# Optimization experiments

Measured on AMD Instinct MI355X. Metric: run time of the kernel, lower is better.

Reference implementation:

```python
import jax, jax.numpy as jnp
import numpy as np

NUM_HEADS = 16
HIDDEN = 1024
B, S = 2, 2048


def setup_inputs() -> dict:
    key = jax.random.key(0)
    ks = jax.random.split(key, 14)
    D = HIDDEN
    scale = 1.0 / np.sqrt(D)
    inp = {
        "query": jax.random.normal(ks[0], (B, S, D), jnp.float32),
        "key_in": jax.random.normal(ks[1], (B, S, D), jnp.float32),
        "value": jax.random.normal(ks[2], (B, S, D), jnp.float32),
        "group_prob": jax.random.uniform(ks[3], (B, S, S), jnp.float32),
        "mask": jax.random.randint(ks[4], (B, S, S), 0, 2, jnp.int32),
        "wq_k": jax.random.normal(ks[5], (D, D), jnp.float32) * scale,
        "wq_b": jnp.zeros((D,), jnp.float32),
        "wk_k": jax.random.normal(ks[6], (D, D), jnp.float32) * scale,
        "wk_b": jnp.zeros((D,), jnp.float32),
        "wv_k": jax.random.normal(ks[7], (D, D), jnp.float32) * scale,
        "wv_b": jnp.zeros((D,), jnp.float32),
        "wo_k": jax.random.normal(ks[8], (D, D), jnp.float32) * scale,
        "wo_b": jnp.zeros((D,), jnp.float32),
    }
    return inp


def _split_heads(x, H):
    b, s, d = x.shape
    return x.reshape(b, s, H, d // H).transpose(0, 2, 1, 3)  # (B,H,S,dh)


def reference(query, key_in, value, group_prob, mask,
              wq_k, wq_b, wk_k, wk_b, wv_k, wv_b, wo_k, wo_b):
    H = NUM_HEADS
    dh = query.shape[-1] // H
    q = _split_heads(query @ wq_k + wq_b, H)
    k = _split_heads(key_in @ wk_k + wk_b, H)
    v = _split_heads(value @ wv_k + wv_b, H)
    # scaled dot-product logits (B,H,Sq,Sk)
    logits = jnp.einsum('bhqd,bhkd->bhqk', q, k) / jnp.sqrt(jnp.asarray(dh, q.dtype))
    neg = (1.0 - mask.astype(q.dtype)) * -1e9
    logits = logits + neg[:, None, :, :]
    attn = jax.nn.softmax(logits, axis=-1)
    # Tree Transformer modulation: post-softmax elementwise scale by group_prob
    attn = attn * group_prob[:, None, :, :]
    out = jnp.einsum('bhqk,bhkd->bhqd', attn, v)
    out = out.transpose(0, 2, 1, 3).reshape(query.shape[0], -1, H * dh)
    return out @ wo_k + wo_b
```

## Files before the change

### kernel.cpp

```cpp
#include <hip/hip_runtime.h>
#include <hip/hip_bf16.h>
#include <stdint.h>

#define B_ 2
#define S_ 2048
#define D_ 1024
#define H_ 16
#define DH 64

typedef __attribute__((ext_vector_type(4))) float f32x4;
typedef __attribute__((ext_vector_type(8))) short s16x8;
typedef __attribute__((ext_vector_type(4))) short s16x4;

__device__ inline short f2bf(float f) {
  union { float f; unsigned u; } v; v.f = f;
  unsigned r = (v.u + 0x7fffu + ((v.u >> 16) & 1u)) >> 16;
  return (short)r;
}

__device__ inline float bfbits_lo(unsigned u) {
  union { unsigned x; float f; } v; v.x = u << 16; return v.f;
}
__device__ inline float bfbits_hi(unsigned u) {
  union { unsigned x; float f; } v; v.x = u & 0xffff0000u; return v.f;
}

__device__ inline float exp2v(float x) {
  float r; asm("v_exp_f32 %0, %1" : "=v"(r) : "v"(x)); return r;
}
__device__ inline unsigned cvtpk(float a, float b) {
  unsigned r; asm("v_cvt_pk_bf16_f32 %0, %1, %2" : "=v"(r) : "v"(a), "v"(b));
  return r;
}

__global__ __launch_bounds__(256) void cvt3_f32_bf16(const float* __restrict__ a,
                                                     const float* __restrict__ b,
                                                     const float* __restrict__ c,
                                                     short* oa, short* ob, short* oc,
                                                     int n) {
  int z = blockIdx.y;
  const float* in = z == 0 ? a : (z == 1 ? b : c);
  short* out = z == 0 ? oa : (z == 1 ? ob : oc);
  int i = (blockIdx.x * 256 + threadIdx.x) * 4;
  if (i < n) {
    float4 v = *(const float4*)(in + i);
    s16x4 o;
    o.x = f2bf(v.x); o.y = f2bf(v.y); o.z = f2bf(v.z); o.w = f2bf(v.w);
    *(s16x4*)(out + i) = o;
  }
}

__global__ __launch_bounds__(256) void fuse_mgp(const int* __restrict__ mask,
                                                const float* __restrict__ gp,
                                                short* __restrict__ mgp, int n) {
  int i = (blockIdx.x * 256 + threadIdx.x) * 4;
  if (i < n) {
    int4 m = *(const int4*)(mask + i);
    float4 g = *(const float4*)(gp + i);
    short b0 = f2bf(g.x); if (!b0) b0 = (short)0x0080;
    short b1 = f2bf(g.y); if (!b1) b1 = (short)0x0080;
    short b2 = f2bf(g.z); if (!b2) b2 = (short)0x0080;
    short b3 = f2bf(g.w); if (!b3) b3 = (short)0x0080;
    s16x4 o;
    o.x = m.x ? b0 : 0;
    o.y = m.y ? b1 : 0;
    o.z = m.z ? b2 : 0;
    o.w = m.w ? b3 : 0;
    *(s16x4*)(mgp + i) = o;
  }
}

__global__ __launch_bounds__(256) void transpose_cvt4(
    const float* __restrict__ i0, const float* __restrict__ i1,
    const float* __restrict__ i2, const float* __restrict__ i3,
    short* o0, short* o1, short* o2, short* o3) {
  int z = blockIdx.z;
  const float* in = z == 0 ? i0 : (z == 1 ? i1 : (z == 2 ? i2 : i3));
  short* out = z == 0 ? o0 : (z == 1 ? o1 : (z == 2 ? o2 : o3));
  __shared__ float tile[32][33];
  int bx = blockIdx.x, by = blockIdx.y;
  int x = bx * 32 + threadIdx.x;
#pragma unroll
  for (int i = 0; i < 32; i += 8) {
    int y = by * 32 + threadIdx.y + i;
    tile[threadIdx.y + i][threadIdx.x] = in[(size_t)y * D_ + x];
  }
  __syncthreads();
  int ox = by * 32 + threadIdx.x;
#pragma unroll
  for (int i = 0; i < 32; i += 8) {
    int oy = bx * 32 + threadIdx.y + i;
    out[(size_t)oy * D_ + ox] = f2bf(tile[threadIdx.x][threadIdx.y + i]);
  }
}

__device__ inline void gload_lds16(const void* g, void* l) {
  __builtin_amdgcn_global_load_lds(
      (const __attribute__((address_space(1))) unsigned*)g,
      (__attribute__((address_space(3))) unsigned*)l, 16, 0, 0);
}

#define BM 128
#define BN 128
#define BK 32

__global__ __launch_bounds__(256) void gemm_bt3(
    const short* __restrict__ A0, const short* __restrict__ A1, const short* __restrict__ A2,
    const short* __restrict__ Bt0, const short* __restrict__ Bt1, const short* __restrict__ Bt2,
    const float* __restrict__ bs0, const float* __restrict__ bs1, const float* __restrict__ bs2,
    void* C0, void* C1, void* C2,
    short* __restrict__ vtout, int vtmode,
    int M, int N, int K, int f32out, float os0, float os1, float os2) {
  int z = blockIdx.y;
  const short* A = z == 0 ? A0 : (z == 1 ? A1 : A2);
  const short* Bt = z == 0 ? Bt0 : (z == 1 ? Bt1 : Bt2);
  const float* bias = z == 0 ? bs0 : (z == 1 ? bs1 : bs2);
  void* C = z == 0 ? C0 : (z == 1 ? C1 : C2);
  float oscale = z == 0 ? os0 : (z == 1 ? os1 : os2);

  __shared__ __align__(16) short As[BM * BK];
  __shared__ __align__(16) short Bs[BN * BK];
  int tid = threadIdx.x;
  int lane = tid & 63, wave = tid >> 6;
  int l15 = lane & 15, l4 = lane >> 4;
  int ntn = N / BN;
  int bid = blockIdx.x;
  bid = ((bid & 7) << 5) | (bid >> 3);
  int bm = bid / ntn, bn = bid % ntn;
  int row0 = bm * BM, col0 = bn * BN;
  int wm = (wave >> 1) * 64, wn = (wave & 1) * 64;

  f32x4 acc[4][4] = {};

  for (int k0 = 0; k0 < K; k0 += BK) {
    __syncthreads();
#pragma unroll
    for (int it = 0; it < 2; ++it) {
      int ch = it * 256 + tid;
      int r = ch >> 2, c = (ch & 3) * 8;
      int ldsbase = (it * 256 + wave * 64) * 8;
      gload_lds16(A + (size_t)(row0 + r) * K + k0 + c, &As[ldsbase]);
      gload_lds16(Bt + (size_t)(col0 + r) * K + k0 + c, &Bs[ldsbase]);
    }
    __syncthreads();
    s16x8 af[4], bf[4];
#pragma unroll
    for (int mf = 0; mf < 4; ++mf)
      af[mf] = *(const s16x8*)&As[(wm + mf * 16 + l15) * BK + l4 * 8];
#pragma unroll
    for (int nf = 0; nf < 4; ++nf)
      bf[nf] = *(const s16x8*)&Bs[(wn + nf * 16 + l15) * BK + l4 * 8];
#pragma unroll
    for (int mf = 0; mf < 4; ++mf)
#pragma unroll
      for (int nf = 0; nf < 4; ++nf)
        acc[mf][nf] = __builtin_amdgcn_mfma_f32_16x16x32_bf16(af[mf], bf[nf],
                                                              acc[mf][nf], 0, 0, 0);
  }

  if (vtmode && z == 2) {
    int b = row0 >> 11;
    int h = (col0 + wn) >> 6;
    int sbase = (row0 & (S_ - 1)) + wm + l4 * 4;
    short* vtb = vtout + ((size_t)(b * H_ + h) * DH) * S_;
#pragma unroll
    for (int nf = 0; nf < 4; ++nf) {
      int dh = nf * 16 + l15;
      float bv = bias[col0 + wn + dh];
#pragma unroll
      for (int mf = 0; mf < 4; ++mf) {
        uint2 o;
        o.x = cvtpk(acc[mf][nf][0] + bv, acc[mf][nf][1] + bv);
        o.y = cvtpk(acc[mf][nf][2] + bv, acc[mf][nf][3] + bv);
        *(uint2*)&vtb[(size_t)dh * S_ + sbase + mf * 16] = o;
      }
    }
    return;
  }

#pragma unroll
  for (int nf = 0; nf < 4; ++nf) {
    int gcol = col0 + wn + nf * 16 + l15;
    float bv = bias[gcol];
#pragma unroll
    for (int mf = 0; mf < 4; ++mf) {
#pragma unroll
      for (int r = 0; r < 4; ++r) {
        int grow = row0 + wm + mf * 16 + l4 * 4 + r;
        float v = (acc[mf][nf][r] + bv) * oscale;
        if (f32out)
          ((float*)C)[(size_t)grow * N + gcol] = v;
        else
          ((short*)C)[(size_t)grow * N + gcol] = f2bf(v);
      }
    }
  }
}

#define QB 128
#define NB 64
#define NTILES (S_ / NB)
#define M0_SHIFT 12.0f

__global__ __launch_bounds__(256, 3) void attn_fused(const short* __restrict__ Qp,
                                                     const short* __restrict__ Kp,
                                                     const short* __restrict__ VT,
                                                     const short* __restrict__ MGP,
                                                     short* __restrict__ ctx) {
  __shared__ __align__(16) short Ks[2][64 * 64];
  __shared__ __align__(16) short Vs[2][64 * 64];
  __shared__ __align__(16) short Ps[4][32 * 64];

  int tid = threadIdx.x, lane = tid & 63, wave = tid >> 6;
  int l15 = lane & 15, l4 = lane >> 4;
  int q0 = blockIdx.x * QB;
  int bh = blockIdx.y;
  int b = bh >> 4, h = bh & 15;
  int wq = wave * 32;

  const short* Qbase = Qp + (size_t)b * S_ * D_ + (size_t)h * DH;
  const short* Kbase = Kp + (size_t)b * S_ * D_ + (size_t)h * DH;
  const short* Vbase = VT + (size_t)(b * H_ + h) * DH * S_;
  const short* Mrow0 = MGP + (size_t)b * S_ * S_ + (size_t)(q0 + wq + l15) * S_ + l4 * 4;
  const short* Mrow1 = Mrow0 + (size_t)16 * S_;

  int i0 = tid, i1 = 256 + tid;
  int r0 = i0 >> 3, c0 = (i0 & 7) ^ (r0 & 7);
  int r1 = i1 >> 3, c1 = (i1 & 7) ^ (r1 & 7);
  int ldsA = wave * 512;
  int ldsB = 2048 + wave * 512;

#define STAGE(kv0, buf)                                                       \
  do {                                                                        \
    gload_lds16(Kbase + (size_t)((kv0) + r0) * D_ + c0 * 8, &Ks[buf][ldsA]);  \
    gload_lds16(Kbase + (size_t)((kv0) + r1) * D_ + c1 * 8, &Ks[buf][ldsB]);  \
    gload_lds16(Vbase + (size_t)r0 * S_ + (kv0) + c0 * 8, &Vs[buf][ldsA]);    \
    gload_lds16(Vbase + (size_t)r1 * S_ + (kv0) + c1 * 8, &Vs[buf][ldsB]);    \
  } while (0)

  s16x8 qf[2][2];
#pragma unroll
  for (int mf = 0; mf < 2; ++mf)
#pragma unroll
    for (int ks = 0; ks < 2; ++ks)
      qf[mf][ks] = *(const s16x8*)(Qbase + (size_t)(q0 + wq + mf * 16 + l15) * D_ +
                                   ks * 32 + l4 * 8);

  float lsum[2] = {0.f, 0.f};
  f32x4 oacc[2][4] = {};

  STAGE(0, 0);

  int q7 = l15 & 7;
  short* Pw = &Ps[wave][0];
  int prow[2] = {l15 * 64, (16 + l15) * 64};

  for (int t = 0; t < NTILES; ++t) {
    int buf = t & 1;
    int kvt = t * NB;

    uint2 g2[2][4];
#pragma unroll
    for (int nf = 0; nf < 4; ++nf) {
      g2[0][nf] = *(const uint2*)(Mrow0 + kvt + nf * 16);
      g2[1][nf] = *(const uint2*)(Mrow1 + kvt + nf * 16);
    }
    __builtin_amdgcn_sched_barrier(0);
    if (t + 1 < NTILES) {
      STAGE((t + 1) * NB, buf ^ 1);
      __builtin_amdgcn_sched_barrier(0);
      asm volatile("s_waitcnt vmcnt(12)" ::: "memory");
    } else {
      __builtin_amdgcn_sched_barrier(0);
      asm volatile("s_waitcnt vmcnt(8)" ::: "memory");
    }
    __builtin_amdgcn_s_barrier();
    __builtin_amdgcn_sched_barrier(0);

    f32x4 sacc[2][4] = {};
    __builtin_amdgcn_s_setprio(1);
#pragma unroll
    for (int nf = 0; nf < 4; ++nf) {
      int R = nf * 16 + l15;
#pragma unroll
      for (int ks = 0; ks < 2; ++ks) {
        s16x8 kf = *(const s16x8*)&Ks[buf][R * 64 + (((ks * 4 + l4) ^ q7) * 8)];
#pragma unroll
        for (int mf = 0; mf < 2; ++mf)
          sacc[mf][nf] = __builtin_amdgcn_mfma_f32_16x16x32_bf16(kf, qf[mf][ks],
                                                                 sacc[mf][nf], 0, 0, 0);
      }
    }
    __builtin_amdgcn_s_setprio(0);

    float ee[2][4][4];
#pragma unroll
    for (int mf = 0; mf < 2; ++mf)
#pragma unroll
      for (int nf = 0; nf < 4; ++nf)
#pragma unroll
        for (int r = 0; r < 4; ++r)
          ee[mf][nf][r] = exp2v(sacc[mf][nf][r] - M0_SHIFT);

    if (t + 1 < NTILES)
      asm volatile("s_waitcnt vmcnt(4)" ::: "memory");
    else
      asm volatile("s_waitcnt vmcnt(0)" ::: "memory");
    __builtin_amdgcn_sched_barrier(0);

#pragma unroll
    for (int mf = 0; mf < 2; ++mf) {
#pragma unroll
      for (int nf = 0; nf < 4; ++nf) {
        float gv0 = bfbits_lo(g2[mf][nf].x), gv1 = bfbits_hi(g2[mf][nf].x);
        float gv2 = bfbits_lo(g2[mf][nf].y), gv3 = bfbits_hi(g2[mf][nf].y);
        float e0 = ee[mf][nf][0], e1 = ee[mf][nf][1];
        float e2 = ee[mf][nf][2], e3 = ee[mf][nf][3];
        lsum[mf] += (gv0 != 0.f) ? e0 : 0.f;
        lsum[mf] += (gv1 != 0.f) ? e1 : 0.f;
        lsum[mf] += (gv2 != 0.f) ? e2 : 0.f;
        lsum[mf] += (gv3 != 0.f) ? e3 : 0.f;
        uint2 wp;
        wp.x = cvtpk(e0 * gv0, e1 * gv1);
        wp.y = cvtpk(e2 * gv2, e3 * gv3);
        int gr = ((nf * 2 + (l4 >> 1)) ^ q7) * 8 + (l4 & 1) * 4;
        *(uint2*)&Pw[prow[mf] + gr] = wp;
      }
    }

    __builtin_amdgcn_s_setprio(1);
#pragma unroll
    for (int ks = 0; ks < 2; ++ks) {
      s16x8 pa[2];
#pragma unroll
      for (int mf = 0; mf < 2; ++mf)
        pa[mf] = *(const s16x8*)&Pw[prow[mf] + (((ks * 4 + l4) ^ q7) * 8)];
#pragma unroll
      for (int df = 0; df < 4; ++df) {
        s16x8 vf = *(const s16x8*)&Vs[buf][(df * 16 + l15) * 64 +
                                           (((ks * 4 + l4) ^ q7) * 8)];
#pragma unroll
        for (int mf = 0; mf < 2; ++mf)
          oacc[mf][df] = __builtin_amdgcn_mfma_f32_16x16x32_bf16(vf, pa[mf],
                                                                 oacc[mf][df], 0, 0, 0);
      }
    }
    __builtin_amdgcn_s_setprio(0);

    asm volatile("s_waitcnt lgkmcnt(0)" ::: "memory");
    __builtin_amdgcn_s_barrier();
  }
#undef STAGE

#pragma unroll
  for (int mf = 0; mf < 2; ++mf) {
    float ls = lsum[mf];
    ls += __shfl_xor(ls, 16);
    ls += __shfl_xor(ls, 32);
    float inv = 1.f / ls;
    short* crow = ctx + ((size_t)(b * S_ + q0 + wq + mf * 16 + l15)) * D_ + h * DH;
#pragma unroll
    for (int df = 0; df < 4; ++df) {
      uint2 o;
      o.x = cvtpk(oacc[mf][df][0] * inv, oacc[mf][df][1] * inv);
      o.y = cvtpk(oacc[mf][df][2] * inv, oacc[mf][df][3] * inv);
      *(uint2*)(crow + df * 16 + l4 * 4) = o;
    }
  }
}

extern "C" void kernel_launch(void* const* d_in, const int* in_sizes, int n_in,
                              void* d_out, int out_size, void* d_ws, size_t ws_size,
                              hipStream_t stream) {
  const float* query = (const float*)d_in[0];
  const float* key_in = (const float*)d_in[1];
  const float* value = (const float*)d_in[2];
  const float* group_prob = (const float*)d_in[3];
  const int* mask = (const int*)d_in[4];
  const float* wq_k = (const float*)d_in[5];
  const float* wq_b = (const float*)d_in[6];
  const float* wk_k = (const float*)d_in[7];
  const float* wk_b = (const float*)d_in[8];
  const float* wv_k = (const float*)d_in[9];
  const float* wv_b = (const float*)d_in[10];
  const float* wo_k = (const float*)d_in[11];
  const float* wo_b = (const float*)d_in[12];
  float* out = (float*)d_out;

  short* ws = (short*)d_ws;
  const size_t NT = (size_t)B_ * S_ * D_;
  short* qbf = ws;
  short* kbf = qbf + NT;
  short* vbf = kbf + NT;
  short* wqt = vbf + NT;
  short* wkt = wqt + (size_t)D_ * D_;
  short* wvt = wkt + (size_t)D_ * D_;
  short* wot = wvt + (size_t)D_ * D_;
  short* qp = wot + (size_t)D_ * D_;
  short* kp = qp + NT;
  short* vt = kp + NT;
  short* ctx = vt + NT;
  short* mgp = ws;

  int nblk = (int)(NT / 4 / 256);
  cvt3_f32_bf16<<<dim3(nblk, 3), 256, 0, stream>>>(query, key_in, value,
                                                   qbf, kbf, vbf, (int)NT);

  dim3 tb(32, 8);
  transpose_cvt4<<<dim3(D_ / 32, D_ / 32, 4), tb, 0, stream>>>(
      wq_k, wk_k, wv_k, wo_k, wqt, wkt, wvt, wot);

  int M = B_ * S_;
  int gblocks = (M / BM) * (D_ / BN);
  const float QSCALE = 0.125f * 1.4426950408889634f;
  gemm_bt3<<<dim3(gblocks, 3), 256, 0, stream>>>(
      qbf, kbf, vbf, wqt, wkt, wvt, wq_b, wk_b, wv_b, qp, kp, nullptr,
      vt, 1, M, D_, D_, 0, QSCALE, 1.0f, 1.0f);

  int nmg = B_ * S_ * S_;
  fuse_mgp<<<nmg / 4 / 256, 256, 0, stream>>>(mask, group_prob, mgp, nmg);

  dim3 ag(S_ / QB, B_ * H_);
  attn_fused<<<ag, 256, 0, stream>>>(qp, kp, vt, mgp, ctx);

  gemm_bt3<<<dim3(gblocks, 1), 256, 0, stream>>>(
      ctx, ctx, ctx, wot, wot, wot, wo_b, wo_b, wo_b, out, out, out,
      nullptr, 0, M, D_, D_, 1, 1.0f, 1.0f, 1.0f);
}
```

Baseline: 175.8 us.

## Fuse fp32-to-bf16 input conversion into QKV GEMM and co-schedule mask fusion

Removes the separate input conversion kernel: the QKV GEMM now loads fp32 activations straight into LDS with an XOR swizzle and converts them to bf16 in registers before the MFMA. The mask/group_prob fusion runs as a fourth grid slice of the same launch, so it overlaps with the GEMM work and one launch disappears. The output GEMM becomes its own specialised kernel. In exchange the A tile in LDS is twice as large and each tile pays conversion instructions. The mgp slice only has gblocks blocks grid-striding over 8M elements, so it may become a long tail.

```diff
diff --git a/kernel.cpp b/kernel.cpp
--- a/kernel.cpp
+++ b/kernel.cpp
@@ -31,43 +31,6 @@
 __device__ inline unsigned cvtpk(float a, float b) {
   unsigned r; asm("v_cvt_pk_bf16_f32 %0, %1, %2" : "=v"(r) : "v"(a), "v"(b));
   return r;
-}
-
-__global__ __launch_bounds__(256) void cvt3_f32_bf16(const float* __restrict__ a,
-                                                     const float* __restrict__ b,
-                                                     const float* __restrict__ c,
-                                                     short* oa, short* ob, short* oc,
-                                                     int n) {
-  int z = blockIdx.y;
-  const float* in = z == 0 ? a : (z == 1 ? b : c);
-  short* out = z == 0 ? oa : (z == 1 ? ob : oc);
-  int i = (blockIdx.x * 256 + threadIdx.x) * 4;
-  if (i < n) {
-    float4 v = *(const float4*)(in + i);
-    s16x4 o;
-    o.x = f2bf(v.x); o.y = f2bf(v.y); o.z = f2bf(v.z); o.w = f2bf(v.w);
-    *(s16x4*)(out + i) = o;
-  }
-}
-
-__global__ __launch_bounds__(256) void fuse_mgp(const int* __restrict__ mask,
-                                                const float* __restrict__ gp,
-                                                short* __restrict__ mgp, int n) {
-  int i = (blockIdx.x * 256 + threadIdx.x) * 4;
-  if (i < n) {
-    int4 m = *(const int4*)(mask + i);
-    float4 g = *(const float4*)(gp + i);
-    short b0 = f2bf(g.x); if (!b0) b0 = (short)0x0080;
-    short b1 = f2bf(g.y); if (!b1) b1 = (short)0x0080;
-    short b2 = f2bf(g.z); if (!b2) b2 = (short)0x0080;
-    short b3 = f2bf(g.w); if (!b3) b3 = (short)0x0080;
-    s16x4 o;
-    o.x = m.x ? b0 : 0;
-    o.y = m.y ? b1 : 0;
-    o.z = m.z ? b2 : 0;
-    o.w = m.w ? b3 : 0;
-    *(s16x4*)(mgp + i) = o;
-  }
 }
 
 __global__ __launch_bounds__(256) void transpose_cvt4(
@@ -104,20 +67,135 @@
 #define BN 128
 #define BK 32
 
-__global__ __launch_bounds__(256) void gemm_bt3(
-    const short* __restrict__ A0, const short* __restrict__ A1, const short* __restrict__ A2,
+__global__ __launch_bounds__(256) void gemm_qkv(
+    const float* __restrict__ A0, const float* __restrict__ A1, const float* __restrict__ A2,
     const short* __restrict__ Bt0, const short* __restrict__ Bt1, const short* __restrict__ Bt2,
     const float* __restrict__ bs0, const float* __restrict__ bs1, const float* __restrict__ bs2,
-    void* C0, void* C1, void* C2,
-    short* __restrict__ vtout, int vtmode,
-    int M, int N, int K, int f32out, float os0, float os1, float os2) {
+    short* __restrict__ Cq, short* __restrict__ Ck, short* __restrict__ vtout,
+    const int* __restrict__ mask, const float* __restrict__ gp,
+    short* __restrict__ mgpout, int nmg,
+    int M, int N, int K, float os0) {
   int z = blockIdx.y;
-  const short* A = z == 0 ? A0 : (z == 1 ? A1 : A2);
+  if (z == 3) {
+    int i = (blockIdx.x * 256 + threadIdx.x) * 4;
+    int stride = gridDim.x * 256 * 4;
+    for (; i < nmg; i += stride) {
+      int4 m = *(const int4*)(mask + i);
+      float4 g = *(const float4*)(gp + i);
+      short b0 = f2bf(g.x); if (!b0) b0 = (short)0x0080;
+      short b1 = f2bf(g.y); if (!b1) b1 = (short)0x0080;
+      short b2 = f2bf(g.z); if (!b2) b2 = (short)0x0080;
+      short b3 = f2bf(g.w); if (!b3) b3 = (short)0x0080;
+      s16x4 o;
+      o.x = m.x ? b0 : 0;
+      o.y = m.y ? b1 : 0;
+      o.z = m.z ? b2 : 0;
+      o.w = m.w ? b3 : 0;
+      *(s16x4*)(mgpout + i) = o;
+    }
+    return;
+  }
+  const float* A = z == 0 ? A0 : (z == 1 ? A1 : A2);
   const short* Bt = z == 0 ? Bt0 : (z == 1 ? Bt1 : Bt2);
   const float* bias = z == 0 ? bs0 : (z == 1 ? bs1 : bs2);
-  void* C = z == 0 ? C0 : (z == 1 ? C1 : C2);
-  float oscale = z == 0 ? os0 : (z == 1 ? os1 : os2);
-
+  float oscale = z == 0 ? os0 : 1.0f;
+
+  __shared__ __align__(16) float As[BM * BK];
+  __shared__ __align__(16) short Bs[BN * BK];
+  int tid = threadIdx.x;
+  int lane = tid & 63, wave = tid >> 6;
+  int l15 = lane & 15, l4 = lane >> 4;
+  int ntn = N / BN;
+  int bid = blockIdx.x;
+  bid = ((bid & 7) << 5) | (bid >> 3);
+  int bm = bid / ntn, bn = bid % ntn;
+  int row0 = bm * BM, col0 = bn * BN;
+  int wm = (wave >> 1) * 64, wn = (wave & 1) * 64;
+  int q7 = l15 & 7;
+
+  f32x4 acc[4][4] = {};
+
+  for (int k0 = 0; k0 < K; k0 += BK) {
+    __syncthreads();
+#pragma unroll
+    for (int it = 0; it < 2; ++it) {
+      int ch = it * 256 + tid;
+      int r = ch >> 2, c = (ch & 3) * 8;
+      int ldsbase = (it * 256 + wave * 64) * 8;
+      gload_lds16(Bt + (size_t)(col0 + r) * K + k0 + c, &Bs[ldsbase]);
+    }
+#pragma unroll
+    for (int it = 0; it < 4; ++it) {
+      int ch = it * 256 + tid;
+      int r = ch >> 3, g = (ch & 7) ^ (r & 7);
+      int ldsbase = (it * 256 + wave * 64) * 4;
+      gload_lds16(A + (size_t)(row0 + r) * K + k0 + g * 4, &As[ldsbase]);
+    }
+    __syncthreads();
+    s16x8 af[4], bf[4];
+#pragma unroll
+    for (int mf = 0; mf < 4; ++mf) {
+      int row = wm + mf * 16 + l15;
+      f32x4 a0 = *(const f32x4*)&As[row * BK + (((2 * l4) ^ q7) * 4)];
+      f32x4 a1 = *(const f32x4*)&As[row * BK + (((2 * l4 + 1) ^ q7) * 4)];
+      union { unsigned w[4]; s16x8 v; } u;
+      u.w[0] = cvtpk(a0[0], a0[1]);
+      u.w[1] = cvtpk(a0[2], a0[3]);
+      u.w[2] = cvtpk(a1[0], a1[1]);
+      u.w[3] = cvtpk(a1[2], a1[3]);
+      af[mf] = u.v;
+    }
+#pragma unroll
+    for (int nf = 0; nf < 4; ++nf)
+      bf[nf] = *(const s16x8*)&Bs[(wn + nf * 16 + l15) * BK + l4 * 8];
+#pragma unroll
+    for (int mf = 0; mf < 4; ++mf)
+#pragma unroll
+      for (int nf = 0; nf < 4; ++nf)
+        acc[mf][nf] = __builtin_amdgcn_mfma_f32_16x16x32_bf16(af[mf], bf[nf],
+                                                              acc[mf][nf], 0, 0, 0);
+  }
+
+  if (z == 2) {
+    int b = row0 >> 11;
+    int h = (col0 + wn) >> 6;
+    int sbase = (row0 & (S_ - 1)) + wm + l4 * 4;
+    short* vtb = vtout + ((size_t)(b * H_ + h) * DH) * S_;
+#pragma unroll
+    for (int nf = 0; nf < 4; ++nf) {
+      int dh = nf * 16 + l15;
+      float bv = bias[col0 + wn + dh];
+#pragma unroll
+      for (int mf = 0; mf < 4; ++mf) {
+        uint2 o;
+        o.x = cvtpk(acc[mf][nf][0] + bv, acc[mf][nf][1] + bv);
+        o.y = cvtpk(acc[mf][nf][2] + bv, acc[mf][nf][3] + bv);
+        *(uint2*)&vtb[(size_t)dh * S_ + sbase + mf * 16] = o;
+      }
+    }
+    return;
+  }
+
+  short* C = z == 0 ? Cq : Ck;
+#pragma unroll
+  for (int nf = 0; nf < 4; ++nf) {
+    int gcol = col0 + wn + nf * 16 + l15;
+    float bv = bias[gcol];
+#pragma unroll
+    for (int mf = 0; mf < 4; ++mf) {
+#pragma unroll
+      for (int r = 0; r < 4; ++r) {
+        int grow = row0 + wm + mf * 16 + l4 * 4 + r;
+        C[(size_t)grow * N + gcol] = f2bf((acc[mf][nf][r] + bv) * oscale);
+      }
+    }
+  }
+}
+
+__global__ __launch_bounds__(256) void gemm_out(
+    const short* __restrict__ A, const short* __restrict__ Bt,
+    const float* __restrict__ bias, float* __restrict__ C,
+    int M, int N, int K) {
   __shared__ __align__(16) short As[BM * BK];
   __shared__ __align__(16) short Bs[BN * BK];
   int tid = threadIdx.x;
@@ -158,26 +236,6 @@
                                                               acc[mf][nf], 0, 0, 0);
   }
 
-  if (vtmode && z == 2) {
-    int b = row0 >> 11;
-    int h = (col0 + wn) >> 6;
-    int sbase = (row0 & (S_ - 1)) + wm + l4 * 4;
-    short* vtb = vtout + ((size_t)(b * H_ + h) * DH) * S_;
-#pragma unroll
-    for (int nf = 0; nf < 4; ++nf) {
-      int dh = nf * 16 + l15;
-      float bv = bias[col0 + wn + dh];
-#pragma unroll
-      for (int mf = 0; mf < 4; ++mf) {
-        uint2 o;
-        o.x = cvtpk(acc[mf][nf][0] + bv, acc[mf][nf][1] + bv);
-        o.y = cvtpk(acc[mf][nf][2] + bv, acc[mf][nf][3] + bv);
-        *(uint2*)&vtb[(size_t)dh * S_ + sbase + mf * 16] = o;
-      }
-    }
-    return;
-  }
-
 #pragma unroll
   for (int nf = 0; nf < 4; ++nf) {
     int gcol = col0 + wn + nf * 16 + l15;
@@ -187,11 +245,7 @@
 #pragma unroll
       for (int r = 0; r < 4; ++r) {
         int grow = row0 + wm + mf * 16 + l4 * 4 + r;
-        float v = (acc[mf][nf][r] + bv) * oscale;
-        if (f32out)
-          ((float*)C)[(size_t)grow * N + gcol] = v;
-        else
-          ((short*)C)[(size_t)grow * N + gcol] = f2bf(v);
+        C[(size_t)grow * N + gcol] = acc[mf][nf][r] + bv;
       }
     }
   }
@@ -389,10 +443,7 @@
 
   short* ws = (short*)d_ws;
   const size_t NT = (size_t)B_ * S_ * D_;
-  short* qbf = ws;
-  short* kbf = qbf + NT;
-  short* vbf = kbf + NT;
-  short* wqt = vbf + NT;
+  short* wqt = ws;
   short* wkt = wqt + (size_t)D_ * D_;
   short* wvt = wkt + (size_t)D_ * D_;
   short* wot = wvt + (size_t)D_ * D_;
@@ -400,11 +451,7 @@
   short* kp = qp + NT;
   short* vt = kp + NT;
   short* ctx = vt + NT;
-  short* mgp = ws;
-
-  int nblk = (int)(NT / 4 / 256);
-  cvt3_f32_bf16<<<dim3(nblk, 3), 256, 0, stream>>>(query, key_in, value,
-                                                   qbf, kbf, vbf, (int)NT);
+  short* mgp = ctx + NT;
 
   dim3 tb(32, 8);
   transpose_cvt4<<<dim3(D_ / 32, D_ / 32, 4), tb, 0, stream>>>(
@@ -412,18 +459,14 @@
 
   int M = B_ * S_;
   int gblocks = (M / BM) * (D_ / BN);
+  int nmg = B_ * S_ * S_;
   const float QSCALE = 0.125f * 1.4426950408889634f;
-  gemm_bt3<<<dim3(gblocks, 3), 256, 0, stream>>>(
-      qbf, kbf, vbf, wqt, wkt, wvt, wq_b, wk_b, wv_b, qp, kp, nullptr,
-      vt, 1, M, D_, D_, 0, QSCALE, 1.0f, 1.0f);
-
-  int nmg = B_ * S_ * S_;
-  fuse_mgp<<<nmg / 4 / 256, 256, 0, stream>>>(mask, group_prob, mgp, nmg);
+  gemm_qkv<<<dim3(gblocks, 4), 256, 0, stream>>>(
+      query, key_in, value, wqt, wkt, wvt, wq_b, wk_b, wv_b,
+      qp, kp, vt, mask, group_prob, mgp, nmg, M, D_, D_, QSCALE);
 
   dim3 ag(S_ / QB, B_ * H_);
   attn_fused<<<ag, 256, 0, stream>>>(qp, kp, vt, mgp, ctx);
 
-  gemm_bt3<<<dim3(gblocks, 1), 256, 0, stream>>>(
-      ctx, ctx, ctx, wot, wot, wot, wo_b, wo_b, wo_b, out, out, out,
-      nullptr, 0, M, D_, D_, 1, 1.0f, 1.0f, 1.0f);
-}
+  gemm_out<<<gblocks, 256, 0, stream>>>(ctx, wot, wo_b, out, M, D_, D_);
+}
```

Measured after the change: 179.1 us. Within noise of the previous version (+1.9%).
